# Optimization experiments

Measured on AMD Instinct MI355X. Metric: run time of the kernel, lower is better.

The kernel has to match this reference:

```python
import jax, jax.numpy as jnp
import numpy as np
import math

HEAD_DIM = 64

def setup_inputs() -> dict:
    key = jax.random.key(0)
    kq, kk, kv = jax.random.split(key, 3)
    B, H, S, D = 2, 16, 2048, HEAD_DIM
    Q = jax.random.normal(kq, (B, H, S, D), dtype=jnp.float32)
    K = jax.random.normal(kk, (B, H, S, D), dtype=jnp.float32)
    V = jax.random.normal(kv, (B, H, S, D), dtype=jnp.float32)
    mask = jnp.ones((B, S), dtype=jnp.float32)
    return {"Q": Q, "K": K, "V": V, "mask": mask}

def reference(Q, K, V, mask):
    # dot: [B, H, S, S]
    dot = jnp.einsum('bhqd,bhkd->bhqk', Q, K) / math.sqrt(HEAD_DIM)
    # additive mask: -1e6 where mask == 0 (mask broadcast over heads and query dim)
    dot = dot - 1000000.0 * (1.0 - mask[:, None, None, :])
    attn = jax.nn.softmax(dot, axis=-1)
    # dropout_prob = 0 -> identity
    X = jnp.einsum('bhqk,bhkd->bhqd', attn, V)
    return X
```

## Files before the change

### kernel.cpp

```cpp
#include <hip/hip_runtime.h>
#include <hip/hip_fp16.h>
#include <stdint.h>


#define S_LEN   2048
#define DHEAD   64
#define NTILE   32
#define CEXP    9.0f
#define SCL2E   0.18033688011112042f
#define L2E     1.4426950408889634f

typedef __attribute__((ext_vector_type(4))) float    f32x4;
typedef __attribute__((ext_vector_type(2))) _Float16 f16x2;
typedef __attribute__((ext_vector_type(4))) _Float16 f16x4;
typedef __attribute__((ext_vector_type(8))) _Float16 f16x8;
typedef __attribute__((ext_vector_type(2))) __fp16   hf16x2;

static __device__ __forceinline__ float exp2_fast(float x) {
#if __has_builtin(__builtin_amdgcn_exp2f)
  return __builtin_amdgcn_exp2f(x);
#else
  float r;
  asm("v_exp_f32 %0, %1" : "=v"(r) : "v"(x));
  return r;
#endif
}

static __device__ __forceinline__ hf16x2 pkh(float a, float b) {
  return __builtin_amdgcn_cvt_pkrtz(a, b);
}
static __device__ __forceinline__ f16x2 h2f(hf16x2 h) {
  union { hf16x2 i; f16x2 o; } u; u.i = h; return u.o;
}

#define GLDS16(g, l)                                                  \
  __builtin_amdgcn_global_load_lds(                                   \
      (const __attribute__((address_space(1))) void*)(g),             \
      (__attribute__((address_space(3))) void*)(l), 16, 0, 0)

__global__ __launch_bounds__(256) void prep(
    const float* __restrict__ K, const float* __restrict__ V,
    const float* __restrict__ Mk, _Float16* __restrict__ Kswz,
    _Float16* __restrict__ Vg, float* __restrict__ madd_g) {
  const int gb = blockIdx.x;
  if (gb < 2048) {
    const int idx = gb * 256 + threadIdx.x;
    const int c  = idx & 7;
    const int kv = (idx >> 3) & 2047;
    const int bh = idx >> 14;
    const float* src = K + ((size_t)bh * S_LEN + kv) * DHEAD + c * 8;
    float4 a = *(const float4*)(src);
    float4 d = *(const float4*)(src + 4);
    union { f16x2 h[4]; f16x8 v; } r;
    r.h[0] = h2f(pkh(a.x, a.y)); r.h[1] = h2f(pkh(a.z, a.w));
    r.h[2] = h2f(pkh(d.x, d.y)); r.h[3] = h2f(pkh(d.z, d.w));
    *(f16x8*)(Kswz + ((size_t)bh * S_LEN + kv) * DHEAD + ((c + kv) & 7) * 8) = r.v;
    if (idx < 2 * S_LEN)
      madd_g[idx] = -CEXP - (1.0e6f * L2E) * (1.0f - Mk[idx]);
  } else {
    const int idx = (gb - 2048) * 256 + threadIdx.x;
    const int d  = idx & 63;
    const int g  = (idx >> 6) & 15;
    const int j  = (idx >> 10) & 31;
    const int bh = idx >> 15;
    const float* src = V + ((size_t)bh * S_LEN + j * 64 + g * 4) * DHEAD + d;
    float v0 = src[0], v1 = src[64], v2 = src[128], v3 = src[192];
    union { f16x2 h[2]; f16x4 v; } r;
    r.h[0] = h2f(pkh(v0, v1)); r.h[1] = h2f(pkh(v2, v3));
    *(f16x4*)(Vg + (size_t)idx * 4) = r.v;
  }
}

__global__ __launch_bounds__(256, 2) void attn_ws(
    const float* __restrict__ Q, const _Float16* __restrict__ Kswz,
    const _Float16* __restrict__ Vg, const float* __restrict__ madd_g,
    float* __restrict__ O) {
  __shared__ __align__(16) _Float16 smem[28672];

  const int tid  = threadIdx.x;
  const int lane = tid & 63;
  const int wave = tid >> 6;
  const int quad = lane >> 4;
  const int x    = lane & 15;

  const int blk  = blockIdx.x;
  const int bh   = (blk & 7) | (((blk >> 3) & 3) << 3);
  const int qblk = blk >> 5;
  const int b    = bh >> 4;

  const size_t base = (size_t)bh * S_LEN * DHEAD;
  const float*    Qb = Q + base;
  const _Float16* Kb = Kswz + base;
  const _Float16* Vb = Vg + base;
  const float*    Mb = madd_g + b * S_LEN;
  float* Ob = O + base;

  float* const mbase = (float*)(smem + 8192);

  const int q0 = qblk * 128 + wave * 16 + x;
  f16x8 qf[2][2];
#pragma unroll
  for (int u = 0; u < 2; ++u) {
    const float* qp = Qb + (size_t)(q0 + u * 64) * DHEAD + quad * 8;
#pragma unroll
    for (int kb = 0; kb < 2; ++kb) {
      float4 a = *(const float4*)(qp + kb * 32);
      float4 c = *(const float4*)(qp + kb * 32 + 4);
      union { f16x2 h[4]; f16x8 v; } r;
      r.h[0] = h2f(pkh(a.x * SCL2E, a.y * SCL2E));
      r.h[1] = h2f(pkh(a.z * SCL2E, a.w * SCL2E));
      r.h[2] = h2f(pkh(c.x * SCL2E, c.y * SCL2E));
      r.h[3] = h2f(pkh(c.z * SCL2E, c.w * SCL2E));
      qf[u][kb] = r.v;
    }
  }

  auto prefetch = [&](int p, int bi) {
    const _Float16* ks = Kb + (size_t)p * 4096 + tid * 8;
    _Float16* kd = smem + bi * 4096 + tid * 8;
    GLDS16(ks,        kd);
    GLDS16(ks + 2048, kd + 2048);
    if (tid < 16)
      GLDS16(Mb + p * 64 + tid * 4, mbase + bi * 64 + tid * 4);
  };

  const _Float16* vlane = Vb + 256 * quad + 4 * x;

  f32x4 xacc[2][4];
#pragma unroll
  for (int u = 0; u < 2; ++u)
#pragma unroll
    for (int m = 0; m < 4; ++m) xacc[u][m] = (f32x4){0.f, 0.f, 0.f, 0.f};
  float lsum[2] = {0.0f, 0.0f};
  const hf16x2 one2 = {(__fp16)1.0f, (__fp16)1.0f};

  prefetch(0, 0);
  __syncthreads();

  for (int p = 0; p < NTILE; ++p) {
    const int cur = p & 1;

    const _Float16* vp = vlane + (size_t)p * 4096;
    f16x4 vf[4][4];
#pragma unroll
    for (int t = 0; t < 4; ++t)
#pragma unroll
      for (int m = 0; m < 4; ++m)
        vf[t][m] = *(const f16x4*)(vp + t * 1024 + m * 64);
    __builtin_amdgcn_sched_barrier(0);

    if (p + 1 < NTILE) prefetch(p + 1, cur ^ 1);

    const _Float16* k0 = smem + cur * 4096 + x * 64 + ((quad + x) & 7) * 8;
    const _Float16* k1 = smem + cur * 4096 + x * 64 + ((quad + 4 + x) & 7) * 8;
    const float*    mp = mbase + cur * 64 + quad * 4;
    f16x4 pf[2][4];
#pragma unroll
    for (int t = 0; t < 4; ++t) {
      f16x8 ka0 = *(const f16x8*)(k0 + t * 1024);
      f16x8 ka1 = *(const f16x8*)(k1 + t * 1024);
      f32x4 mi = *(const f32x4*)(mp + t * 16);
#pragma unroll
      for (int u = 0; u < 2; ++u) {
        f32x4 st = __builtin_amdgcn_mfma_f32_16x16x32_f16(ka0, qf[u][0], mi, 0, 0, 0);
        st = __builtin_amdgcn_mfma_f32_16x16x32_f16(ka1, qf[u][1], st, 0, 0, 0);
        hf16x2 h0 = pkh(exp2_fast(st.x), exp2_fast(st.y));
        hf16x2 h1 = pkh(exp2_fast(st.z), exp2_fast(st.w));
#if __has_builtin(__builtin_amdgcn_fdot2)
        lsum[u] = __builtin_amdgcn_fdot2(h0, one2, lsum[u], false);
        lsum[u] = __builtin_amdgcn_fdot2(h1, one2, lsum[u], false);
#else
        f16x2 a0 = h2f(h0), a1 = h2f(h1);
        lsum[u] += (float)a0.x + (float)a0.y + (float)a1.x + (float)a1.y;
#endif
        union { f16x2 h[2]; f16x4 v; } r;
        r.h[0] = h2f(h0);
        r.h[1] = h2f(h1);
        pf[u][t] = r.v;
      }
    }
#pragma unroll
    for (int m = 0; m < 4; ++m) {
      f32x4 x0 = xacc[0][m];
      f32x4 x1 = xacc[1][m];
#pragma unroll
      for (int t = 0; t < 4; ++t) {
        x0 = __builtin_amdgcn_mfma_f32_16x16x16f16(vf[t][m], pf[0][t], x0, 0, 0, 0);
        x1 = __builtin_amdgcn_mfma_f32_16x16x16f16(vf[t][m], pf[1][t], x1, 0, 0, 0);
      }
      xacc[0][m] = x0;
      xacc[1][m] = x1;
    }
    __syncthreads();
  }

#pragma unroll
  for (int u = 0; u < 2; ++u) {
    float l = lsum[u];
    l += __shfl_xor(l, 16, 64);
    l += __shfl_xor(l, 32, 64);
    const float rl = 1.0f / l;
    float* op = Ob + (size_t)(q0 + u * 64) * DHEAD;
#pragma unroll
    for (int m = 0; m < 4; ++m) {
      float4 o;
      o.x = xacc[u][m].x * rl; o.y = xacc[u][m].y * rl;
      o.z = xacc[u][m].z * rl; o.w = xacc[u][m].w * rl;
      *(float4*)(op + m * 16 + quad * 4) = o;
    }
  }
}

extern "C" void kernel_launch(void* const* d_in, const int* in_sizes, int n_in,
                              void* d_out, int out_size, void* d_ws, size_t ws_size,
                              hipStream_t stream) {
  const float* Q = (const float*)d_in[0];
  const float* K = (const float*)d_in[1];
  const float* V = (const float*)d_in[2];
  const float* M = (const float*)d_in[3];
  float* O = (float*)d_out;

  _Float16* Kswz = (_Float16*)d_ws;
  _Float16* Vg   = Kswz + 4194304;
  float*    madd = (float*)((char*)d_ws + 16777216);
  hipLaunchKernelGGL(prep, dim3(6144), dim3(256), 0, stream, K, V, M, Kswz, Vg, madd);
  hipLaunchKernelGGL(attn_ws, dim3(512), dim3(256), 0, stream, Q, Kswz, Vg, madd, O);
}
```

Measured before the change: 142.3 us.

## Load K tiles directly into registers in MFMA fragment layout, drop LDS staging

The prep kernel now writes K in a per-lane fragment order so each lane can load its MFMA operands straight from global memory. The attention kernel drops the shared-memory double buffer, the global_load_lds prefetch and the per-tile __syncthreads, and instead double-buffers K fragments in registers through a ping-pong unrolled loop. The mask add moves from the MFMA accumulator init to a vector add before exp2. This removes LDS traffic and block-wide barriers but raises register pressure and makes each of the four waves fetch K from global/L2 separately.

```diff
diff --git a/kernel.cpp b/kernel.cpp
--- a/kernel.cpp
+++ b/kernel.cpp
@@ -33,28 +33,26 @@
   union { hf16x2 i; f16x2 o; } u; u.i = h; return u.o;
 }
 
-#define GLDS16(g, l)                                                  \
-  __builtin_amdgcn_global_load_lds(                                   \
-      (const __attribute__((address_space(1))) void*)(g),             \
-      (__attribute__((address_space(3))) void*)(l), 16, 0, 0)
-
 __global__ __launch_bounds__(256) void prep(
     const float* __restrict__ K, const float* __restrict__ V,
-    const float* __restrict__ Mk, _Float16* __restrict__ Kswz,
+    const float* __restrict__ Mk, _Float16* __restrict__ K2,
     _Float16* __restrict__ Vg, float* __restrict__ madd_g) {
   const int gb = blockIdx.x;
   if (gb < 2048) {
     const int idx = gb * 256 + threadIdx.x;
-    const int c  = idx & 7;
-    const int kv = (idx >> 3) & 2047;
+    const int x  = idx & 15;
+    const int c  = (idx >> 4) & 7;
+    const int t  = (idx >> 7) & 3;
+    const int p  = (idx >> 9) & 31;
     const int bh = idx >> 14;
+    const int kv = p * 64 + t * 16 + x;
     const float* src = K + ((size_t)bh * S_LEN + kv) * DHEAD + c * 8;
     float4 a = *(const float4*)(src);
     float4 d = *(const float4*)(src + 4);
     union { f16x2 h[4]; f16x8 v; } r;
     r.h[0] = h2f(pkh(a.x, a.y)); r.h[1] = h2f(pkh(a.z, a.w));
     r.h[2] = h2f(pkh(d.x, d.y)); r.h[3] = h2f(pkh(d.z, d.w));
-    *(f16x8*)(Kswz + ((size_t)bh * S_LEN + kv) * DHEAD + ((c + kv) & 7) * 8) = r.v;
+    *(f16x8*)(K2 + (size_t)idx * 8) = r.v;
     if (idx < 2 * S_LEN)
       madd_g[idx] = -CEXP - (1.0e6f * L2E) * (1.0f - Mk[idx]);
   } else {
@@ -72,11 +70,9 @@
 }
 
 __global__ __launch_bounds__(256, 2) void attn_ws(
-    const float* __restrict__ Q, const _Float16* __restrict__ Kswz,
+    const float* __restrict__ Q, const _Float16* __restrict__ K2,
     const _Float16* __restrict__ Vg, const float* __restrict__ madd_g,
     float* __restrict__ O) {
-  __shared__ __align__(16) _Float16 smem[28672];
-
   const int tid  = threadIdx.x;
   const int lane = tid & 63;
   const int wave = tid >> 6;
@@ -90,12 +86,11 @@
 
   const size_t base = (size_t)bh * S_LEN * DHEAD;
   const float*    Qb = Q + base;
-  const _Float16* Kb = Kswz + base;
-  const _Float16* Vb = Vg + base;
-  const float*    Mb = madd_g + b * S_LEN;
   float* Ob = O + base;
 
-  float* const mbase = (float*)(smem + 8192);
+  const _Float16* klane = K2 + base + quad * 128 + x * 8;
+  const _Float16* vlane = Vg + base + 256 * quad + 4 * x;
+  const float*    mlane = madd_g + b * S_LEN + quad * 4;
 
   const int q0 = qblk * 128 + wave * 16 + x;
   f16x8 qf[2][2];
@@ -115,16 +110,18 @@
     }
   }
 
-  auto prefetch = [&](int p, int bi) {
-    const _Float16* ks = Kb + (size_t)p * 4096 + tid * 8;
-    _Float16* kd = smem + bi * 4096 + tid * 8;
-    GLDS16(ks,        kd);
-    GLDS16(ks + 2048, kd + 2048);
-    if (tid < 16)
-      GLDS16(Mb + p * 64 + tid * 4, mbase + bi * 64 + tid * 4);
+  f16x8 kA[4][2], kB[4][2];
+  f16x4 vv[4][4];
+  f32x4 mi[4];
+
+  auto loadK = [&](int p, f16x8 (&kf)[4][2]) {
+#pragma unroll
+    for (int t = 0; t < 4; ++t) {
+      const _Float16* kp = klane + (size_t)p * 4096 + t * 1024;
+      kf[t][0] = *(const f16x8*)(kp);
+      kf[t][1] = *(const f16x8*)(kp + 512);
+    }
   };
-
-  const _Float16* vlane = Vb + 256 * quad + 4 * x;
 
   f32x4 xacc[2][4];
 #pragma unroll
@@ -133,39 +130,31 @@
     for (int m = 0; m < 4; ++m) xacc[u][m] = (f32x4){0.f, 0.f, 0.f, 0.f};
   float lsum[2] = {0.0f, 0.0f};
   const hf16x2 one2 = {(__fp16)1.0f, (__fp16)1.0f};
-
-  prefetch(0, 0);
-  __syncthreads();
-
-  for (int p = 0; p < NTILE; ++p) {
-    const int cur = p & 1;
-
-    const _Float16* vp = vlane + (size_t)p * 4096;
-    f16x4 vf[4][4];
+  const f32x4 zf = (f32x4){0.f, 0.f, 0.f, 0.f};
+
+  loadK(0, kA);
+
+  auto step = [&](int p, f16x8 (&kCur)[4][2], f16x8 (&kNxt)[4][2]) {
 #pragma unroll
     for (int t = 0; t < 4; ++t)
+      mi[t] = *(const f32x4*)(mlane + p * 64 + t * 16);
+    if (p + 1 < NTILE) loadK(p + 1, kNxt);
+#pragma unroll
+    for (int t = 0; t < 4; ++t)
 #pragma unroll
       for (int m = 0; m < 4; ++m)
-        vf[t][m] = *(const f16x4*)(vp + t * 1024 + m * 64);
-    __builtin_amdgcn_sched_barrier(0);
-
-    if (p + 1 < NTILE) prefetch(p + 1, cur ^ 1);
-
-    const _Float16* k0 = smem + cur * 4096 + x * 64 + ((quad + x) & 7) * 8;
-    const _Float16* k1 = smem + cur * 4096 + x * 64 + ((quad + 4 + x) & 7) * 8;
-    const float*    mp = mbase + cur * 64 + quad * 4;
+        vv[t][m] = *(const f16x4*)(vlane + (size_t)p * 4096 + t * 1024 + m * 64);
+
     f16x4 pf[2][4];
 #pragma unroll
     for (int t = 0; t < 4; ++t) {
-      f16x8 ka0 = *(const f16x8*)(k0 + t * 1024);
-      f16x8 ka1 = *(const f16x8*)(k1 + t * 1024);
-      f32x4 mi = *(const f32x4*)(mp + t * 16);
+      const f32x4 miv = mi[t];
 #pragma unroll
       for (int u = 0; u < 2; ++u) {
-        f32x4 st = __builtin_amdgcn_mfma_f32_16x16x32_f16(ka0, qf[u][0], mi, 0, 0, 0);
-        st = __builtin_amdgcn_mfma_f32_16x16x32_f16(ka1, qf[u][1], st, 0, 0, 0);
-        hf16x2 h0 = pkh(exp2_fast(st.x), exp2_fast(st.y));
-        hf16x2 h1 = pkh(exp2_fast(st.z), exp2_fast(st.w));
+        f32x4 st = __builtin_amdgcn_mfma_f32_16x16x32_f16(kCur[t][0], qf[u][0], zf, 0, 0, 0);
+        st = __builtin_amdgcn_mfma_f32_16x16x32_f16(kCur[t][1], qf[u][1], st, 0, 0, 0);
+        hf16x2 h0 = pkh(exp2_fast(st.x + miv.x), exp2_fast(st.y + miv.y));
+        hf16x2 h1 = pkh(exp2_fast(st.z + miv.z), exp2_fast(st.w + miv.w));
 #if __has_builtin(__builtin_amdgcn_fdot2)
         lsum[u] = __builtin_amdgcn_fdot2(h0, one2, lsum[u], false);
         lsum[u] = __builtin_amdgcn_fdot2(h1, one2, lsum[u], false);
@@ -185,13 +174,17 @@
       f32x4 x1 = xacc[1][m];
 #pragma unroll
       for (int t = 0; t < 4; ++t) {
-        x0 = __builtin_amdgcn_mfma_f32_16x16x16f16(vf[t][m], pf[0][t], x0, 0, 0, 0);
-        x1 = __builtin_amdgcn_mfma_f32_16x16x16f16(vf[t][m], pf[1][t], x1, 0, 0, 0);
+        x0 = __builtin_amdgcn_mfma_f32_16x16x16f16(vv[t][m], pf[0][t], x0, 0, 0, 0);
+        x1 = __builtin_amdgcn_mfma_f32_16x16x16f16(vv[t][m], pf[1][t], x1, 0, 0, 0);
       }
       xacc[0][m] = x0;
       xacc[1][m] = x1;
     }
-    __syncthreads();
+  };
+
+  for (int pp = 0; pp < NTILE / 2; ++pp) {
+    step(2 * pp,     kA, kB);
+    step(2 * pp + 1, kB, kA);
   }
 
 #pragma unroll
@@ -220,9 +213,9 @@
   const float* M = (const float*)d_in[3];
   float* O = (float*)d_out;
 
-  _Float16* Kswz = (_Float16*)d_ws;
-  _Float16* Vg   = Kswz + 4194304;
+  _Float16* K2   = (_Float16*)d_ws;
+  _Float16* Vg   = K2 + 4194304;
   float*    madd = (float*)((char*)d_ws + 16777216);
-  hipLaunchKernelGGL(prep, dim3(6144), dim3(256), 0, stream, K, V, M, Kswz, Vg, madd);
-  hipLaunchKernelGGL(attn_ws, dim3(512), dim3(256), 0, stream, Q, Kswz, Vg, madd, O);
-}
+  hipLaunchKernelGGL(prep, dim3(6144), dim3(256), 0, stream, K, V, M, K2, Vg, madd);
+  hipLaunchKernelGGL(attn_ws, dim3(512), dim3(256), 0, stream, Q, K2, Vg, madd, O);
+}
```

After: 153.1 us. 1.08x slower.

## Software-pipeline QK^T of next tile with PV of previous tile

Applied to the files above, without the earlier changes.

Restructures the main loop so that the QK^T MFMAs, exp2 and P packing for tile i are interleaved with the PV MFMAs for tile i-1, using two ping-pong P register sets and a manual 2x unroll with prologue and epilogue. This lets the matrix core work and the transcendental and VALU work from independent tiles overlap instead of running back-to-back. Shared memory is also trimmed to the actually used size, which could raise occupancy. The cost is more live registers (two P sets plus V fragments), which may cause spills or lower occupancy.

```diff
diff --git a/kernel.cpp b/kernel.cpp
--- a/kernel.cpp
+++ b/kernel.cpp
@@ -5,7 +5,6 @@
 
 #define S_LEN   2048
 #define DHEAD   64
-#define NTILE   32
 #define CEXP    9.0f
 #define SCL2E   0.18033688011112042f
 #define L2E     1.4426950408889634f
@@ -31,6 +30,18 @@
 }
 static __device__ __forceinline__ f16x2 h2f(hf16x2 h) {
   union { hf16x2 i; f16x2 o; } u; u.i = h; return u.o;
+}
+
+static __device__ __forceinline__ float sum2(float acc, hf16x2 h0, hf16x2 h1) {
+#if __has_builtin(__builtin_amdgcn_fdot2)
+  const hf16x2 one2 = {(__fp16)1.0f, (__fp16)1.0f};
+  acc = __builtin_amdgcn_fdot2(h0, one2, acc, false);
+  acc = __builtin_amdgcn_fdot2(h1, one2, acc, false);
+  return acc;
+#else
+  f16x2 a0 = h2f(h0), a1 = h2f(h1);
+  return acc + (float)a0.x + (float)a0.y + (float)a1.x + (float)a1.y;
+#endif
 }
 
 #define GLDS16(g, l)                                                  \
@@ -71,11 +82,62 @@
   }
 }
 
+#define QK_T(bi, t, pf)                                                       \
+  {                                                                           \
+    f16x8 ka0 = *(const f16x8*)(k0base + (bi) * 4096 + (t) * 1024);           \
+    f16x8 ka1 = *(const f16x8*)(k1base + (bi) * 4096 + (t) * 1024);           \
+    f32x4 mi  = *(const f32x4*)(mpbase + (bi) * 64 + (t) * 16);               \
+    _Pragma("unroll")                                                         \
+    for (int u = 0; u < 2; ++u) {                                             \
+      f32x4 st = __builtin_amdgcn_mfma_f32_16x16x32_f16(ka0, qf[u][0], mi, 0, 0, 0); \
+      st = __builtin_amdgcn_mfma_f32_16x16x32_f16(ka1, qf[u][1], st, 0, 0, 0);       \
+      hf16x2 h0 = pkh(exp2_fast(st.x), exp2_fast(st.y));                      \
+      hf16x2 h1 = pkh(exp2_fast(st.z), exp2_fast(st.w));                      \
+      lsum[u] = sum2(lsum[u], h0, h1);                                        \
+      union { f16x2 h[2]; f16x4 v; } r;                                       \
+      r.h[0] = h2f(h0);                                                       \
+      r.h[1] = h2f(h1);                                                       \
+      pf[u][t] = r.v;                                                         \
+    }                                                                         \
+  }
+
+#define PV_M(m, pf)                                                           \
+  {                                                                           \
+    f32x4 x0 = xacc[0][m];                                                    \
+    f32x4 x1 = xacc[1][m];                                                    \
+    _Pragma("unroll")                                                         \
+    for (int t = 0; t < 4; ++t) {                                             \
+      x0 = __builtin_amdgcn_mfma_f32_16x16x16f16(vv[t][m], pf[0][t], x0, 0, 0, 0); \
+      x1 = __builtin_amdgcn_mfma_f32_16x16x16f16(vv[t][m], pf[1][t], x1, 0, 0, 0); \
+    }                                                                         \
+    xacc[0][m] = x0;                                                          \
+    xacc[1][m] = x1;                                                          \
+  }
+
+#define VLOAD(p)                                                              \
+  _Pragma("unroll")                                                           \
+  for (int t = 0; t < 4; ++t)                                                 \
+    _Pragma("unroll")                                                         \
+    for (int m = 0; m < 4; ++m)                                               \
+      vv[t][m] = *(const f16x4*)(vlane + (size_t)(p) * 4096 + t * 1024 + m * 64);
+
+#define PITER(i, bi, pfN, pfO)                                                \
+  {                                                                           \
+    VLOAD((i) - 1);                                                           \
+    __builtin_amdgcn_sched_barrier(0);                                        \
+    if ((i) < 31) stage((i) + 1, ((i) + 1) & 1);                              \
+    QK_T(bi, 0, pfN); PV_M(0, pfO);                                           \
+    QK_T(bi, 1, pfN); PV_M(1, pfO);                                           \
+    QK_T(bi, 2, pfN); PV_M(2, pfO);                                           \
+    QK_T(bi, 3, pfN); PV_M(3, pfO);                                           \
+    __syncthreads();                                                          \
+  }
+
 __global__ __launch_bounds__(256, 2) void attn_ws(
     const float* __restrict__ Q, const _Float16* __restrict__ Kswz,
     const _Float16* __restrict__ Vg, const float* __restrict__ madd_g,
     float* __restrict__ O) {
-  __shared__ __align__(16) _Float16 smem[28672];
+  __shared__ __align__(16) _Float16 smem[8448];
 
   const int tid  = threadIdx.x;
   const int lane = tid & 63;
@@ -115,7 +177,7 @@
     }
   }
 
-  auto prefetch = [&](int p, int bi) {
+  auto stage = [&](int p, int bi) {
     const _Float16* ks = Kb + (size_t)p * 4096 + tid * 8;
     _Float16* kd = smem + bi * 4096 + tid * 8;
     GLDS16(ks,        kd);
@@ -124,7 +186,10 @@
       GLDS16(Mb + p * 64 + tid * 4, mbase + bi * 64 + tid * 4);
   };
 
-  const _Float16* vlane = Vb + 256 * quad + 4 * x;
+  const _Float16* vlane  = Vb + 256 * quad + 4 * x;
+  const _Float16* k0base = smem + x * 64 + ((quad + x) & 7) * 8;
+  const _Float16* k1base = smem + x * 64 + ((quad + 4 + x) & 7) * 8;
+  const float*    mpbase = mbase + quad * 4;
 
   f32x4 xacc[2][4];
 #pragma unroll
@@ -132,67 +197,25 @@
 #pragma unroll
     for (int m = 0; m < 4; ++m) xacc[u][m] = (f32x4){0.f, 0.f, 0.f, 0.f};
   float lsum[2] = {0.0f, 0.0f};
-  const hf16x2 one2 = {(__fp16)1.0f, (__fp16)1.0f};
-
-  prefetch(0, 0);
+
+  f16x4 pfA[2][4], pfB[2][4];
+  f16x4 vv[4][4];
+
+  stage(0, 0);
   __syncthreads();
-
-  for (int p = 0; p < NTILE; ++p) {
-    const int cur = p & 1;
-
-    const _Float16* vp = vlane + (size_t)p * 4096;
-    f16x4 vf[4][4];
-#pragma unroll
-    for (int t = 0; t < 4; ++t)
-#pragma unroll
-      for (int m = 0; m < 4; ++m)
-        vf[t][m] = *(const f16x4*)(vp + t * 1024 + m * 64);
-    __builtin_amdgcn_sched_barrier(0);
-
-    if (p + 1 < NTILE) prefetch(p + 1, cur ^ 1);
-
-    const _Float16* k0 = smem + cur * 4096 + x * 64 + ((quad + x) & 7) * 8;
-    const _Float16* k1 = smem + cur * 4096 + x * 64 + ((quad + 4 + x) & 7) * 8;
-    const float*    mp = mbase + cur * 64 + quad * 4;
-    f16x4 pf[2][4];
-#pragma unroll
-    for (int t = 0; t < 4; ++t) {
-      f16x8 ka0 = *(const f16x8*)(k0 + t * 1024);
-      f16x8 ka1 = *(const f16x8*)(k1 + t * 1024);
-      f32x4 mi = *(const f32x4*)(mp + t * 16);
-#pragma unroll
-      for (int u = 0; u < 2; ++u) {
-        f32x4 st = __builtin_amdgcn_mfma_f32_16x16x32_f16(ka0, qf[u][0], mi, 0, 0, 0);
-        st = __builtin_amdgcn_mfma_f32_16x16x32_f16(ka1, qf[u][1], st, 0, 0, 0);
-        hf16x2 h0 = pkh(exp2_fast(st.x), exp2_fast(st.y));
-        hf16x2 h1 = pkh(exp2_fast(st.z), exp2_fast(st.w));
-#if __has_builtin(__builtin_amdgcn_fdot2)
-        lsum[u] = __builtin_amdgcn_fdot2(h0, one2, lsum[u], false);
-        lsum[u] = __builtin_amdgcn_fdot2(h1, one2, lsum[u], false);
-#else
-        f16x2 a0 = h2f(h0), a1 = h2f(h1);
-        lsum[u] += (float)a0.x + (float)a0.y + (float)a1.x + (float)a1.y;
-#endif
-        union { f16x2 h[2]; f16x4 v; } r;
-        r.h[0] = h2f(h0);
-        r.h[1] = h2f(h1);
-        pf[u][t] = r.v;
-      }
-    }
-#pragma unroll
-    for (int m = 0; m < 4; ++m) {
-      f32x4 x0 = xacc[0][m];
-      f32x4 x1 = xacc[1][m];
-#pragma unroll
-      for (int t = 0; t < 4; ++t) {
-        x0 = __builtin_amdgcn_mfma_f32_16x16x16f16(vf[t][m], pf[0][t], x0, 0, 0, 0);
-        x1 = __builtin_amdgcn_mfma_f32_16x16x16f16(vf[t][m], pf[1][t], x1, 0, 0, 0);
-      }
-      xacc[0][m] = x0;
-      xacc[1][m] = x1;
-    }
-    __syncthreads();
-  }
+  stage(1, 1);
+  QK_T(0, 0, pfA); QK_T(0, 1, pfA); QK_T(0, 2, pfA); QK_T(0, 3, pfA);
+  __syncthreads();
+
+#pragma unroll 1
+  for (int ii = 0; ii < 15; ++ii) {
+    const int i = 2 * ii + 1;
+    PITER(i,     1, pfB, pfA);
+    PITER(i + 1, 0, pfA, pfB);
+  }
+  PITER(31, 1, pfB, pfA);
+  VLOAD(31);
+  PV_M(0, pfB); PV_M(1, pfB); PV_M(2, pfB); PV_M(3, pfB);
 
 #pragma unroll
   for (int u = 0; u < 2; ++u) {
```

After: 150.1 us. 5.5% more time.
